# Kernel optimization log

Measured on AMD Instinct MI355X. Metric: run time of the kernel, lower is better.

Reference implementation:

```python
import jax, jax.numpy as jnp
import numpy as np
import math

B = 16384
INPUT = 2048
HIDDEN = 2048
PROJ = 1024


def setup_inputs() -> dict:
    key = jax.random.key(0)
    ks = jax.random.split(key, 20)
    stdv = 1.0 / math.sqrt(PROJ)
    u = lambda k, shape: jax.random.uniform(k, shape, jnp.float32, -stdv, stdv)
    return {
        "x_t": jax.random.normal(ks[0], (B, INPUT), jnp.float32),
        "h_t": jax.random.normal(ks[1], (B, PROJ), jnp.float32),
        "c_t": jax.random.normal(ks[2], (B, HIDDEN), jnp.float32),
        "weight_if_x": u(ks[3], (INPUT, 2 * HIDDEN)),
        "weight_if_h": u(ks[4], (PROJ, 2 * HIDDEN)),
        "weight_if_c": u(ks[5], (HIDDEN, 2 * HIDDEN)),
        "bias_i": u(ks[6], (HIDDEN,)),
        "bias_f": u(ks[7], (HIDDEN,)),
        "weight_c_x": u(ks[8], (INPUT, HIDDEN)),
        "weight_c_h": u(ks[9], (PROJ, HIDDEN)),
        "bias_c": u(ks[10], (HIDDEN,)),
        "weight_o_x": u(ks[11], (INPUT, PROJ)),
        "weight_o_h": u(ks[12], (PROJ, PROJ)),
        "weight_o_c": u(ks[13], (HIDDEN, PROJ)),
        "bias_o": u(ks[14], (PROJ,)),
        "weight_r_proj": u(ks[15], (HIDDEN, PROJ)),
        "weight_r_x": u(ks[16], (INPUT, PROJ)),
    }


def reference(x_t, h_t, c_t, weight_if_x, weight_if_h, weight_if_c, bias_i, bias_f,
              weight_c_x, weight_c_h, bias_c, weight_o_x, weight_o_h, weight_o_c,
              bias_o, weight_r_proj, weight_r_x):
    # input/forget gates with peephole on c_t: [B, 2*HIDDEN]
    if_gates = x_t @ weight_if_x + h_t @ weight_if_h + c_t @ weight_if_c
    ingate, forgetgate = jnp.split(if_gates, 2, axis=-1)
    ingate = jax.nn.sigmoid(ingate + bias_i)
    forgetgate = jax.nn.sigmoid(forgetgate + bias_f)
    cellgate = jnp.tanh(x_t @ weight_c_x + h_t @ weight_c_h + bias_c)
    c_new = forgetgate * c_t + ingate * cellgate
    # output gate peeps at new cell state
    outgate = jax.nn.sigmoid(x_t @ weight_o_x + h_t @ weight_o_h + c_new @ weight_o_c + bias_o)
    r_t = jnp.tanh(c_new)
    m_t = r_t @ weight_r_proj
    # input_size != proj_size -> project x for the residual connection
    h_new = outgate * (m_t + x_t @ weight_r_x)
    return (h_new, c_new)
```

## Files before the change

kernel.cpp:

```cpp
#include <hip/hip_runtime.h>
#include <hip/hip_bf16.h>
#include <math.h>

typedef unsigned short u16;
typedef __bf16 bf16x8_t __attribute__((ext_vector_type(8)));
typedef float  f32x8_t  __attribute__((ext_vector_type(8)));
typedef float  f32x16_t __attribute__((ext_vector_type(16)));
typedef u16    u16x4_t  __attribute__((ext_vector_type(4)));
typedef u16    u16x8_t  __attribute__((ext_vector_type(8)));

__device__ __forceinline__ u16 f2b(float f) {
  unsigned u = __builtin_bit_cast(unsigned, f);
  u += 0x7fffu + ((u >> 16) & 1u);
  return (u16)(u >> 16);
}
__device__ __forceinline__ float b2f(u16 h) {
  unsigned u = ((unsigned)h) << 16;
  return __builtin_bit_cast(float, u);
}
__device__ __forceinline__ float sigm_(float x) { return 1.0f / (1.0f + __expf(-x)); }
__device__ __forceinline__ float tanh_(float x) { return 1.0f - 2.0f / (__expf(2.0f * x) + 1.0f); }

__device__ __forceinline__ void gload16(const void* g, void* l) {
  __builtin_amdgcn_global_load_lds(
      (__attribute__((address_space(1))) void*)(g),
      (__attribute__((address_space(3))) void*)(l), 16, 0, 0);
}


__global__ void pack_act_kernel(const float* __restrict__ x, const float* __restrict__ h,
                                const float* __restrict__ c, u16* __restrict__ A1p) {
  int mb = blockIdx.x, kt = blockIdx.y, t = threadIdx.x;
  const float* src; int C, ccol;
  if (kt < 64)      { src = x; C = 2048; ccol = kt * 32; }
  else if (kt < 96) { src = h; C = 1024; ccol = (kt - 64) * 32; }
  else              { src = c; C = 2048; ccol = (kt - 96) * 32; }
  const float* s = src + (long)(mb * 256 + t) * C + ccol;
  u16* d = A1p + ((long)(mb * 160 + kt)) * 8192 + t * 8;
#pragma unroll
  for (int p = 0; p < 4; ++p) {
    f32x8_t v = *(const f32x8_t*)(s + p * 8);
    u16x8_t o;
#pragma unroll
    for (int r = 0; r < 8; ++r) o[r] = f2b(v[r]);
    *(u16x8_t*)(d + p * 2048) = o;
  }
}

__global__ void pack_w1_kernel(const float* __restrict__ w_if_x, const float* __restrict__ w_if_h,
                               const float* __restrict__ w_if_c, const float* __restrict__ w_c_x,
                               const float* __restrict__ w_c_h,  const float* __restrict__ w_o_x,
                               const float* __restrict__ w_o_h,  const float* __restrict__ w_r_x,
                               u16* __restrict__ W1tp) {
  int nb = blockIdx.x, kt = blockIdx.y, t = threadIdx.x;
  int n0g = nb * 256;
  const float* src; int N, nl, kl;
  if (n0g < 4096) {
    N = 4096; nl = n0g;
    if (kt < 64)      { src = w_if_x; kl = kt * 32; }
    else if (kt < 96) { src = w_if_h; kl = (kt - 64) * 32; }
    else              { src = w_if_c; kl = (kt - 96) * 32; }
  } else if (n0g < 6144) {
    N = 2048; nl = n0g - 4096;
    if (kt < 64)      { src = w_c_x; kl = kt * 32; }
    else if (kt < 96) { src = w_c_h; kl = (kt - 64) * 32; }
    else return;
  } else if (n0g < 7168) {
    N = 1024; nl = n0g - 6144;
    if (kt < 64)      { src = w_o_x; kl = kt * 32; }
    else if (kt < 96) { src = w_o_h; kl = (kt - 64) * 32; }
    else return;
  } else {
    N = 1024; nl = n0g - 7168;
    if (kt < 64)      { src = w_r_x; kl = kt * 32; }
    else return;
  }
  int n = nl + t;
  float tmp[32];
#pragma unroll
  for (int kk = 0; kk < 32; ++kk)
    tmp[kk] = src[(long)(kl + kk) * N + n];
  u16* d = W1tp + ((long)(nb * 160 + kt)) * 8192 + t * 8;
#pragma unroll
  for (int p = 0; p < 4; ++p) {
    u16x8_t o;
#pragma unroll
    for (int r = 0; r < 8; ++r) o[r] = f2b(tmp[p * 8 + r]);
    *(u16x8_t*)(d + p * 2048) = o;
  }
}

__global__ void pack_w2_kernel(const float* __restrict__ w_o_c,
                               const float* __restrict__ w_r_proj, u16* __restrict__ W2tp) {
  int nb = blockIdx.x, kt = blockIdx.y, t = threadIdx.x;
  const float* src; int nl, kl;
  if (nb < 4) { if (kt >= 64) return; src = w_o_c;    nl = nb * 256;       kl = kt * 32; }
  else        { if (kt < 64)  return; src = w_r_proj; nl = (nb - 4) * 256; kl = (kt - 64) * 32; }
  int n = nl + t;
  float tmp[32];
#pragma unroll
  for (int kk = 0; kk < 32; ++kk)
    tmp[kk] = src[(long)(kl + kk) * 1024 + n];
  u16* d = W2tp + ((long)(nb * 128 + kt)) * 8192 + t * 8;
#pragma unroll
  for (int p = 0; p < 4; ++p) {
    u16x8_t o;
#pragma unroll
    for (int r = 0; r < 8; ++r) o[r] = f2b(tmp[p * 8 + r]);
    *(u16x8_t*)(d + p * 2048) = o;
  }
}

template <int MODE>
__global__ __launch_bounds__(512, 2) void gemm256_kernel(
    const u16* __restrict__ A, const u16* __restrict__ Bt, u16* __restrict__ Cout) {
  constexpr int KTF  = (MODE == 0) ? 160 : 128;
  constexpr int NCOL = (MODE == 0) ? 8192 : 2048;
  constexpr int NBN  = NCOL / 256;
  constexpr int SLOT = 16384;

  __shared__ u16 lds[3 * SLOT];

  int bid = blockIdx.x;
  int cpx = gridDim.x >> 3;
  bid = (bid & 7) * cpx + (bid >> 3);

  int mb = bid / NBN, nb = bid % NBN;
  int m0 = mb * 256, n0 = nb * 256;

  int kt0, NT;
  if (MODE == 0) { kt0 = 0; NT = (nb < 16) ? 160 : ((nb < 28) ? 96 : 64); }
  else           { kt0 = (nb < 4) ? 0 : 64; NT = 64; }

  const int tid  = threadIdx.x;
  const int lane = tid & 63;
  const int wid  = tid >> 6;
  const int wr   = wid >> 2;
  const int wc   = wid & 3;
  const int l31  = lane & 31;
  const int hl   = lane >> 5;

  const int dstg = tid * 8;
  const u16* pA = A  + ((long)(mb * KTF + kt0)) * 8192 + dstg;
  const u16* pB = Bt + ((long)(nb * KTF + kt0)) * 8192 + dstg;

#define STAGE(t, s) do { \
    gload16(pA + (long)(t) * 8192,        &lds[(s) * SLOT + dstg]); \
    gload16(pA + (long)(t) * 8192 + 4096, &lds[(s) * SLOT + dstg + 4096]); \
    gload16(pB + (long)(t) * 8192,        &lds[(s) * SLOT + 8192 + dstg]); \
    gload16(pB + (long)(t) * 8192 + 4096, &lds[(s) * SLOT + 8192 + dstg + 4096]); } while (0)

  const int abase = (wr * 128 + l31) * 8;
  const int bbase = (wc * 64  + l31) * 8;

  f32x16_t acc[4][2];
#pragma unroll
  for (int m = 0; m < 4; ++m)
#pragma unroll
    for (int n = 0; n < 2; ++n)
#pragma unroll
      for (int r = 0; r < 16; ++r) acc[m][n][r] = 0.f;

  STAGE(0, 0); STAGE(1, 1);
  asm volatile("s_waitcnt vmcnt(4)" ::: "memory");
  __builtin_amdgcn_s_barrier();

  int slot = 0, s2 = 2;
  for (int t = 0; t < NT; ++t) {
    const u16* sA = &lds[slot * SLOT];
    const u16* sB = sA + 8192;
    const bool pre = (t + 2 < NT);
    if (pre) STAGE(t + 2, s2);

    bf16x8_t xa[4], xb[4], wa[2], wb[2];
#pragma unroll
    for (int m = 0; m < 4; ++m) {
      xa[m] = *(const bf16x8_t*)&sA[hl * 2048 + abase + m * 256];
      xb[m] = *(const bf16x8_t*)&sA[(2 + hl) * 2048 + abase + m * 256];
    }
#pragma unroll
    for (int n = 0; n < 2; ++n) {
      wa[n] = *(const bf16x8_t*)&sB[hl * 2048 + bbase + n * 256];
      wb[n] = *(const bf16x8_t*)&sB[(2 + hl) * 2048 + bbase + n * 256];
    }

    __builtin_amdgcn_s_setprio(1);
#pragma unroll
    for (int m = 0; m < 4; ++m)
#pragma unroll
      for (int n = 0; n < 2; ++n)
        acc[m][n] = __builtin_amdgcn_mfma_f32_32x32x16_bf16(wa[n], xa[m], acc[m][n], 0, 0, 0);
#pragma unroll
    for (int m = 0; m < 4; ++m)
#pragma unroll
      for (int n = 0; n < 2; ++n)
        acc[m][n] = __builtin_amdgcn_mfma_f32_32x32x16_bf16(wb[n], xb[m], acc[m][n], 0, 0, 0);
    __builtin_amdgcn_s_setprio(0);

    if (pre) asm volatile("s_waitcnt vmcnt(4)" ::: "memory");
    else     asm volatile("s_waitcnt vmcnt(0)" ::: "memory");
    __builtin_amdgcn_s_barrier();

    slot = (slot == 2) ? 0 : slot + 1;
    s2   = (s2   == 2) ? 0 : s2   + 1;
  }
#undef STAGE

  const long rowg = (long)(m0 + wr * 128 + l31);
  const int  colg = n0 + wc * 64 + 4 * hl;
#pragma unroll
  for (int mm = 0; mm < 4; ++mm) {
    long rb = (rowg + mm * 32) * (long)NCOL;
#pragma unroll
    for (int nn = 0; nn < 2; ++nn) {
#pragma unroll
      for (int g = 0; g < 4; ++g) {
        u16x4_t o;
#pragma unroll
        for (int r = 0; r < 4; ++r) o[r] = f2b(acc[mm][nn][g * 4 + r]);
        *(u16x4_t*)&Cout[rb + colg + nn * 32 + g * 8] = o;
      }
    }
  }
}

__global__ void pass2_kernel(const u16* __restrict__ G1, const float* __restrict__ c_t,
                             const float* __restrict__ bias_i, const float* __restrict__ bias_f,
                             const float* __restrict__ bias_c,
                             float* __restrict__ c_new_out, u16* __restrict__ A2p) {
  int mb = blockIdx.x, jg = blockIdx.y, t = threadIdx.x;
  int b = mb * 256 + t;
  int j0 = jg * 32;
  const u16* row = G1 + (long)b * 8192 + j0;
  const float* cp_p = c_t + (long)b * 2048 + j0;
  float* co_p = c_new_out + (long)b * 2048 + j0;
  u16* dc = A2p + ((long)(mb * 128 + jg)) * 8192 + t * 8;
  u16* dr = dc + (long)64 * 8192;

#pragma unroll
  for (int q = 0; q < 4; ++q) {
    u16x8_t ip = *(const u16x8_t*)(row + q * 8);
    u16x8_t fp = *(const u16x8_t*)(row + 2048 + q * 8);
    u16x8_t gp = *(const u16x8_t*)(row + 4096 + q * 8);
    f32x8_t cp = *(const f32x8_t*)(cp_p + q * 8);
    f32x8_t bi = *(const f32x8_t*)(bias_i + j0 + q * 8);
    f32x8_t bf = *(const f32x8_t*)(bias_f + j0 + q * 8);
    f32x8_t bc = *(const f32x8_t*)(bias_c + j0 + q * 8);
    f32x8_t cn;
    u16x8_t cb, rb;
#pragma unroll
    for (int r = 0; r < 8; ++r) {
      float ig = sigm_(b2f(ip[r]) + bi[r]);
      float fg = sigm_(b2f(fp[r]) + bf[r]);
      float g  = tanh_(b2f(gp[r]) + bc[r]);
      float c  = fg * cp[r] + ig * g;
      cn[r] = c;
      cb[r] = f2b(c);
      rb[r] = f2b(tanh_(c));
    }
    *(f32x8_t*)(co_p + q * 8) = cn;
    *(u16x8_t*)(dc + q * 2048) = cb;
    *(u16x8_t*)(dr + q * 2048) = rb;
  }
}

__global__ void pass3_kernel(const u16* __restrict__ G1, const u16* __restrict__ G2,
                             const float* __restrict__ bias_o, float* __restrict__ h_out) {
  long i = (long)blockIdx.x * blockDim.x + threadIdx.x;
  long e = i * 8;
  int b = (int)(e >> 10);
  int j = (int)(e & 1023);
  const u16* row1 = G1 + (long)b * 8192;
  const u16* row2 = G2 + (long)b * 2048;
  u16x8_t ogp = *(const u16x8_t*)(row1 + 6144 + j);
  u16x8_t xrp = *(const u16x8_t*)(row1 + 7168 + j);
  u16x8_t ocg = *(const u16x8_t*)(row2 + j);
  u16x8_t mt  = *(const u16x8_t*)(row2 + 1024 + j);
  f32x8_t bo  = *(const f32x8_t*)(bias_o + j);
  f32x8_t h;
#pragma unroll
  for (int r = 0; r < 8; ++r) {
    float og = sigm_(b2f(ogp[r]) + b2f(ocg[r]) + bo[r]);
    h[r] = og * (b2f(mt[r]) + b2f(xrp[r]));
  }
  *(f32x8_t*)(h_out + (long)b * 1024 + j) = h;
}

extern "C" void kernel_launch(void* const* d_in, const int* in_sizes, int n_in,
                              void* d_out, int out_size, void* d_ws, size_t ws_size,
                              hipStream_t stream) {
  const float* x_t      = (const float*)d_in[0];
  const float* h_t      = (const float*)d_in[1];
  const float* c_t      = (const float*)d_in[2];
  const float* w_if_x   = (const float*)d_in[3];
  const float* w_if_h   = (const float*)d_in[4];
  const float* w_if_c   = (const float*)d_in[5];
  const float* bias_i   = (const float*)d_in[6];
  const float* bias_f   = (const float*)d_in[7];
  const float* w_c_x    = (const float*)d_in[8];
  const float* w_c_h    = (const float*)d_in[9];
  const float* bias_c   = (const float*)d_in[10];
  const float* w_o_x    = (const float*)d_in[11];
  const float* w_o_h    = (const float*)d_in[12];
  const float* w_o_c    = (const float*)d_in[13];
  const float* bias_o   = (const float*)d_in[14];
  const float* w_r_proj = (const float*)d_in[15];
  const float* w_r_x    = (const float*)d_in[16];

  char* ws = (char*)d_ws;
  u16* A1p  = (u16*)(ws);
  u16* W1tp = (u16*)(ws + 167772160L);
  u16* G1   = (u16*)(ws + 251658240L);
  u16* W2tp = (u16*)(ws + 520093696L);
  u16* A2p  = (u16*)(ws);
  u16* G2   = (u16*)(ws + 167772160L);

  float* h_out = (float*)d_out;
  float* c_out = h_out + 16384L * 1024L;

  pack_act_kernel<<<dim3(64, 160), 256, 0, stream>>>(x_t, h_t, c_t, A1p);
  pack_w1_kernel<<<dim3(32, 160), 256, 0, stream>>>(w_if_x, w_if_h, w_if_c, w_c_x, w_c_h,
                                                    w_o_x, w_o_h, w_r_x, W1tp);
  pack_w2_kernel<<<dim3(8, 128), 256, 0, stream>>>(w_o_c, w_r_proj, W2tp);

  gemm256_kernel<0><<<2048, 512, 0, stream>>>(A1p, W1tp, G1);

  pass2_kernel<<<dim3(64, 64), 256, 0, stream>>>(G1, c_t, bias_i, bias_f, bias_c, c_out, A2p);

  gemm256_kernel<1><<<512, 512, 0, stream>>>(A2p, W2tp, G2);

  pass3_kernel<<<8192, 256, 0, stream>>>(G1, G2, bias_o, h_out);
}
```

Measured before the change: 1.569 ms.

## Switch GEMMs to 16x16x32 MFMA and fuse output-gate epilogue into second GEMM

The first GEMM moves from 32x32x16 to 16x16x32 bf16 MFMA tiles with a new LDS read pattern and store layout. The second GEMM is rewritten so each block computes matching 128-column slices of both the o_c peephole product and the r_proj product, keeping them in two accumulator sets. It then applies sigmoid and the residual combine directly into h_out, which removes the G2 intermediate and the separate pass3 kernel. W2 is repacked into the column-group layout this needs. The cost is a deeper K loop per block and more accumulator registers.

```diff
diff --git a/kernel.cpp b/kernel.cpp
--- a/kernel.cpp
+++ b/kernel.cpp
@@ -4,8 +4,8 @@
 
 typedef unsigned short u16;
 typedef __bf16 bf16x8_t __attribute__((ext_vector_type(8)));
+typedef float  f32x4_t  __attribute__((ext_vector_type(4)));
 typedef float  f32x8_t  __attribute__((ext_vector_type(8)));
-typedef float  f32x16_t __attribute__((ext_vector_type(16)));
 typedef u16    u16x4_t  __attribute__((ext_vector_type(4)));
 typedef u16    u16x8_t  __attribute__((ext_vector_type(8)));
 
@@ -91,32 +91,31 @@
 }
 
 __global__ void pack_w2_kernel(const float* __restrict__ w_o_c,
-                               const float* __restrict__ w_r_proj, u16* __restrict__ W2tp) {
-  int nb = blockIdx.x, kt = blockIdx.y, t = threadIdx.x;
-  const float* src; int nl, kl;
-  if (nb < 4) { if (kt >= 64) return; src = w_o_c;    nl = nb * 256;       kl = kt * 32; }
-  else        { if (kt < 64)  return; src = w_r_proj; nl = (nb - 4) * 256; kl = (kt - 64) * 32; }
-  int n = nl + t;
+                               const float* __restrict__ w_r_proj, u16* __restrict__ W2q) {
+  int cg = blockIdx.x, kt = blockIdx.y, t = threadIdx.x;
+  const float* src; int kl;
+  if (kt < 64) { src = w_o_c;    kl = kt * 32; }
+  else         { src = w_r_proj; kl = (kt - 64) * 32; }
+  int n = cg * 128 + t;
   float tmp[32];
 #pragma unroll
   for (int kk = 0; kk < 32; ++kk)
     tmp[kk] = src[(long)(kl + kk) * 1024 + n];
-  u16* d = W2tp + ((long)(nb * 128 + kt)) * 8192 + t * 8;
+  u16* d = W2q + ((long)(cg * 128 + kt)) * 4096 + t * 8;
 #pragma unroll
   for (int p = 0; p < 4; ++p) {
     u16x8_t o;
 #pragma unroll
     for (int r = 0; r < 8; ++r) o[r] = f2b(tmp[p * 8 + r]);
-    *(u16x8_t*)(d + p * 2048) = o;
-  }
-}
-
-template <int MODE>
-__global__ __launch_bounds__(512, 2) void gemm256_kernel(
+    *(u16x8_t*)(d + p * 1024) = o;
+  }
+}
+
+__global__ __launch_bounds__(512, 2) void gemm1_kernel(
     const u16* __restrict__ A, const u16* __restrict__ Bt, u16* __restrict__ Cout) {
-  constexpr int KTF  = (MODE == 0) ? 160 : 128;
-  constexpr int NCOL = (MODE == 0) ? 8192 : 2048;
-  constexpr int NBN  = NCOL / 256;
+  constexpr int KTF  = 160;
+  constexpr int NCOL = 8192;
+  constexpr int NBN  = 32;
   constexpr int SLOT = 16384;
 
   __shared__ u16 lds[3 * SLOT];
@@ -128,21 +127,19 @@
   int mb = bid / NBN, nb = bid % NBN;
   int m0 = mb * 256, n0 = nb * 256;
 
-  int kt0, NT;
-  if (MODE == 0) { kt0 = 0; NT = (nb < 16) ? 160 : ((nb < 28) ? 96 : 64); }
-  else           { kt0 = (nb < 4) ? 0 : 64; NT = 64; }
+  int NT = (nb < 16) ? 160 : ((nb < 28) ? 96 : 64);
 
   const int tid  = threadIdx.x;
   const int lane = tid & 63;
   const int wid  = tid >> 6;
   const int wr   = wid >> 2;
   const int wc   = wid & 3;
-  const int l31  = lane & 31;
-  const int hl   = lane >> 5;
+  const int hl16 = lane >> 4;
+  const int l15  = lane & 15;
 
   const int dstg = tid * 8;
-  const u16* pA = A  + ((long)(mb * KTF + kt0)) * 8192 + dstg;
-  const u16* pB = Bt + ((long)(nb * KTF + kt0)) * 8192 + dstg;
+  const u16* pA = A  + ((long)(mb * KTF)) * 8192 + dstg;
+  const u16* pB = Bt + ((long)(nb * KTF)) * 8192 + dstg;
 
 #define STAGE(t, s) do { \
     gload16(pA + (long)(t) * 8192,        &lds[(s) * SLOT + dstg]); \
@@ -150,16 +147,14 @@
     gload16(pB + (long)(t) * 8192,        &lds[(s) * SLOT + 8192 + dstg]); \
     gload16(pB + (long)(t) * 8192 + 4096, &lds[(s) * SLOT + 8192 + dstg + 4096]); } while (0)
 
-  const int abase = (wr * 128 + l31) * 8;
-  const int bbase = (wc * 64  + l31) * 8;
-
-  f32x16_t acc[4][2];
-#pragma unroll
-  for (int m = 0; m < 4; ++m)
-#pragma unroll
-    for (int n = 0; n < 2; ++n)
-#pragma unroll
-      for (int r = 0; r < 16; ++r) acc[m][n][r] = 0.f;
+  const int aoff = hl16 * 2048 + (wr * 128 + l15) * 8;
+  const int boff = hl16 * 2048 + (wc * 64  + l15) * 8;
+
+  f32x4_t acc[8][4];
+#pragma unroll
+  for (int m = 0; m < 8; ++m)
+#pragma unroll
+    for (int n = 0; n < 4; ++n) acc[m][n] = (f32x4_t){0.f, 0.f, 0.f, 0.f};
 
   STAGE(0, 0); STAGE(1, 1);
   asm volatile("s_waitcnt vmcnt(4)" ::: "memory");
@@ -172,29 +167,18 @@
     const bool pre = (t + 2 < NT);
     if (pre) STAGE(t + 2, s2);
 
-    bf16x8_t xa[4], xb[4], wa[2], wb[2];
-#pragma unroll
-    for (int m = 0; m < 4; ++m) {
-      xa[m] = *(const bf16x8_t*)&sA[hl * 2048 + abase + m * 256];
-      xb[m] = *(const bf16x8_t*)&sA[(2 + hl) * 2048 + abase + m * 256];
-    }
-#pragma unroll
-    for (int n = 0; n < 2; ++n) {
-      wa[n] = *(const bf16x8_t*)&sB[hl * 2048 + bbase + n * 256];
-      wb[n] = *(const bf16x8_t*)&sB[(2 + hl) * 2048 + bbase + n * 256];
-    }
+    bf16x8_t bv[4], av[8];
+#pragma unroll
+    for (int n = 0; n < 4; ++n) bv[n] = *(const bf16x8_t*)&sB[boff + n * 128];
+#pragma unroll
+    for (int m = 0; m < 8; ++m) av[m] = *(const bf16x8_t*)&sA[aoff + m * 128];
 
     __builtin_amdgcn_s_setprio(1);
 #pragma unroll
-    for (int m = 0; m < 4; ++m)
-#pragma unroll
-      for (int n = 0; n < 2; ++n)
-        acc[m][n] = __builtin_amdgcn_mfma_f32_32x32x16_bf16(wa[n], xa[m], acc[m][n], 0, 0, 0);
-#pragma unroll
-    for (int m = 0; m < 4; ++m)
-#pragma unroll
-      for (int n = 0; n < 2; ++n)
-        acc[m][n] = __builtin_amdgcn_mfma_f32_32x32x16_bf16(wb[n], xb[m], acc[m][n], 0, 0, 0);
+    for (int m = 0; m < 8; ++m)
+#pragma unroll
+      for (int n = 0; n < 4; ++n)
+        acc[m][n] = __builtin_amdgcn_mfma_f32_16x16x32_bf16(bv[n], av[m], acc[m][n], 0, 0, 0);
     __builtin_amdgcn_s_setprio(0);
 
     if (pre) asm volatile("s_waitcnt vmcnt(4)" ::: "memory");
@@ -206,20 +190,18 @@
   }
 #undef STAGE
 
-  const long rowg = (long)(m0 + wr * 128 + l31);
-  const int  colg = n0 + wc * 64 + 4 * hl;
-#pragma unroll
-  for (int mm = 0; mm < 4; ++mm) {
-    long rb = (rowg + mm * 32) * (long)NCOL;
-#pragma unroll
-    for (int nn = 0; nn < 2; ++nn) {
-#pragma unroll
-      for (int g = 0; g < 4; ++g) {
-        u16x4_t o;
-#pragma unroll
-        for (int r = 0; r < 4; ++r) o[r] = f2b(acc[mm][nn][g * 4 + r]);
-        *(u16x4_t*)&Cout[rb + colg + nn * 32 + g * 8] = o;
-      }
+  const int rowm = lane & 15;
+  const int col4 = (lane >> 4) * 4;
+#pragma unroll
+  for (int m = 0; m < 8; ++m) {
+    long rg = (long)(m0 + wr * 128 + m * 16 + rowm) * NCOL;
+#pragma unroll
+    for (int n = 0; n < 4; ++n) {
+      int cg = n0 + wc * 64 + n * 16 + col4;
+      u16x4_t o;
+#pragma unroll
+      for (int r = 0; r < 4; ++r) o[r] = f2b(acc[m][n][r]);
+      *(u16x4_t*)&Cout[rg + cg] = o;
     }
   }
 }
@@ -264,26 +246,111 @@
   }
 }
 
-__global__ void pass3_kernel(const u16* __restrict__ G1, const u16* __restrict__ G2,
-                             const float* __restrict__ bias_o, float* __restrict__ h_out) {
-  long i = (long)blockIdx.x * blockDim.x + threadIdx.x;
-  long e = i * 8;
-  int b = (int)(e >> 10);
-  int j = (int)(e & 1023);
-  const u16* row1 = G1 + (long)b * 8192;
-  const u16* row2 = G2 + (long)b * 2048;
-  u16x8_t ogp = *(const u16x8_t*)(row1 + 6144 + j);
-  u16x8_t xrp = *(const u16x8_t*)(row1 + 7168 + j);
-  u16x8_t ocg = *(const u16x8_t*)(row2 + j);
-  u16x8_t mt  = *(const u16x8_t*)(row2 + 1024 + j);
-  f32x8_t bo  = *(const f32x8_t*)(bias_o + j);
-  f32x8_t h;
-#pragma unroll
-  for (int r = 0; r < 8; ++r) {
-    float og = sigm_(b2f(ogp[r]) + b2f(ocg[r]) + bo[r]);
-    h[r] = og * (b2f(mt[r]) + b2f(xrp[r]));
-  }
-  *(f32x8_t*)(h_out + (long)b * 1024 + j) = h;
+__global__ __launch_bounds__(512, 2) void gemm2h_kernel(
+    const u16* __restrict__ A2p, const u16* __restrict__ W2q,
+    const u16* __restrict__ G1, const float* __restrict__ bias_o,
+    float* __restrict__ h_out) {
+  constexpr int SLOT = 12288;
+
+  __shared__ u16 lds[3 * SLOT];
+
+  int bid = blockIdx.x;
+  int cpx = gridDim.x >> 3;
+  bid = (bid & 7) * cpx + (bid >> 3);
+
+  int mb = bid >> 3, cg = bid & 7;
+  int m0 = mb * 256, c0 = cg * 128;
+
+  const int tid  = threadIdx.x;
+  const int lane = tid & 63;
+  const int wid  = tid >> 6;
+  const int wr   = wid >> 1;
+  const int wc   = wid & 1;
+  const int hl16 = lane >> 4;
+  const int l15  = lane & 15;
+
+  const int dstg = tid * 8;
+  const u16* pA = A2p + ((long)(mb * 128)) * 8192 + dstg;
+  const u16* pB = W2q + ((long)(cg * 128)) * 4096 + dstg;
+
+#define STAGE2(t, s) do { \
+    gload16(pA + (long)(t) * 8192,        &lds[(s) * SLOT + dstg]); \
+    gload16(pA + (long)(t) * 8192 + 4096, &lds[(s) * SLOT + dstg + 4096]); \
+    gload16(pB + (long)(t) * 4096,        &lds[(s) * SLOT + 8192 + dstg]); } while (0)
+
+  const int aoff = hl16 * 2048 + (wr * 64 + l15) * 8;
+  const int boff = hl16 * 1024 + (wc * 64 + l15) * 8;
+
+  f32x4_t acc0[4][4], acc1[4][4];
+#pragma unroll
+  for (int m = 0; m < 4; ++m)
+#pragma unroll
+    for (int n = 0; n < 4; ++n) {
+      acc0[m][n] = (f32x4_t){0.f, 0.f, 0.f, 0.f};
+      acc1[m][n] = (f32x4_t){0.f, 0.f, 0.f, 0.f};
+    }
+
+  STAGE2(0, 0); STAGE2(1, 1);
+  asm volatile("s_waitcnt vmcnt(3)" ::: "memory");
+  __builtin_amdgcn_s_barrier();
+
+  int slot = 0, s2 = 2;
+  for (int t = 0; t < 128; ++t) {
+    const u16* sA = &lds[slot * SLOT];
+    const u16* sB = sA + 8192;
+    const bool pre = (t + 2 < 128);
+    if (pre) STAGE2(t + 2, s2);
+
+    bf16x8_t wv[4], av[4];
+#pragma unroll
+    for (int n = 0; n < 4; ++n) wv[n] = *(const bf16x8_t*)&sB[boff + n * 128];
+#pragma unroll
+    for (int m = 0; m < 4; ++m) av[m] = *(const bf16x8_t*)&sA[aoff + m * 128];
+
+    __builtin_amdgcn_s_setprio(1);
+    if (t < 64) {
+#pragma unroll
+      for (int m = 0; m < 4; ++m)
+#pragma unroll
+        for (int n = 0; n < 4; ++n)
+          acc0[m][n] = __builtin_amdgcn_mfma_f32_16x16x32_bf16(wv[n], av[m], acc0[m][n], 0, 0, 0);
+    } else {
+#pragma unroll
+      for (int m = 0; m < 4; ++m)
+#pragma unroll
+        for (int n = 0; n < 4; ++n)
+          acc1[m][n] = __builtin_amdgcn_mfma_f32_16x16x32_bf16(wv[n], av[m], acc1[m][n], 0, 0, 0);
+    }
+    __builtin_amdgcn_s_setprio(0);
+
+    if (pre) asm volatile("s_waitcnt vmcnt(3)" ::: "memory");
+    else     asm volatile("s_waitcnt vmcnt(0)" ::: "memory");
+    __builtin_amdgcn_s_barrier();
+
+    slot = (slot == 2) ? 0 : slot + 1;
+    s2   = (s2   == 2) ? 0 : s2   + 1;
+  }
+#undef STAGE2
+
+#pragma unroll
+  for (int m = 0; m < 4; ++m) {
+    int row = m0 + wr * 64 + m * 16 + l15;
+    const u16* g1r = G1 + (long)row * 8192;
+#pragma unroll
+    for (int n = 0; n < 4; ++n) {
+      int jb = c0 + wc * 64 + n * 16 + 4 * hl16;
+      u16x4_t og = *(const u16x4_t*)(g1r + 6144 + jb);
+      u16x4_t xr = *(const u16x4_t*)(g1r + 7168 + jb);
+      f32x4_t bo = *(const f32x4_t*)(bias_o + jb);
+      f32x4_t h;
+#pragma unroll
+      for (int r = 0; r < 4; ++r) {
+        float ogate = sigm_(acc0[m][n][r] + b2f(og[r]) + bo[r]);
+        h[r] = ogate * (acc1[m][n][r] + b2f(xr[r]));
+      }
+      *(f32x4_t*)&h_out[(long)row * 1024 + jb] = h;
+    }
+  }
 }
 
 extern "C" void kernel_launch(void* const* d_in, const int* in_sizes, int n_in,
@@ -311,9 +378,8 @@
   u16* A1p  = (u16*)(ws);
   u16* W1tp = (u16*)(ws + 167772160L);
   u16* G1   = (u16*)(ws + 251658240L);
-  u16* W2tp = (u16*)(ws + 520093696L);
+  u16* W2q  = (u16*)(ws + 520093696L);
   u16* A2p  = (u16*)(ws);
-  u16* G2   = (u16*)(ws + 167772160L);
 
   float* h_out = (float*)d_out;
   float* c_out = h_out + 16384L * 1024L;
@@ -321,13 +387,11 @@
   pack_act_kernel<<<dim3(64, 160), 256, 0, stream>>>(x_t, h_t, c_t, A1p);
   pack_w1_kernel<<<dim3(32, 160), 256, 0, stream>>>(w_if_x, w_if_h, w_if_c, w_c_x, w_c_h,
                                                     w_o_x, w_o_h, w_r_x, W1tp);
-  pack_w2_kernel<<<dim3(8, 128), 256, 0, stream>>>(w_o_c, w_r_proj, W2tp);
-
-  gemm256_kernel<0><<<2048, 512, 0, stream>>>(A1p, W1tp, G1);
+  pack_w2_kernel<<<dim3(8, 128), 128, 0, stream>>>(w_o_c, w_r_proj, W2q);
+
+  gemm1_kernel<<<2048, 512, 0, stream>>>(A1p, W1tp, G1);
 
   pass2_kernel<<<dim3(64, 64), 256, 0, stream>>>(G1, c_t, bias_i, bias_f, bias_c, c_out, A2p);
 
-  gemm256_kernel<1><<<512, 512, 0, stream>>>(A2p, W2tp, G2);
-
-  pass3_kernel<<<8192, 256, 0, stream>>>(G1, G2, bias_o, h_out);
-}
+  gemm2h_kernel<<<512, 512, 0, stream>>>(A2p, W2q, G1, bias_o, h_out);
+}
```

Measured after the change: 1.492 ms. -4.9%, faster.
